# Kernel tuning notes

Hardware: AMD Instinct MI355X
Metric: run time of the kernel (lower is better)

The kernel has to match this reference:

```python
import jax, jax.numpy as jnp
import numpy as np

L, N, D = 4, 50000, 64        # lookback, n_nodes, gnn_dim
E = 500000                    # n_edges
HID = 256
LN_EPS = 1e-5


def setup_inputs() -> dict:
    key = jax.random.key(0)
    ks = jax.random.split(key, 8)
    h_all = jax.random.normal(ks[0], (L, N, D), dtype=jnp.float32)
    src = jax.random.randint(ks[1], (E,), 0, N, dtype=jnp.int32)
    dst = jax.random.randint(ks[2], (E,), 0, N, dtype=jnp.int32)
    W1 = jax.random.normal(ks[3], (HID, L * 2 * D), dtype=jnp.float32) * (1.0 / np.sqrt(L * 2 * D))
    b1 = jax.random.normal(ks[4], (HID,), dtype=jnp.float32) * 0.01
    W3 = jax.random.normal(ks[5], (1, HID), dtype=jnp.float32) * (1.0 / np.sqrt(HID))
    b3 = jax.random.normal(ks[6], (1,), dtype=jnp.float32) * 0.01
    gamma2 = jnp.ones((HID,), dtype=jnp.float32)
    beta2 = jnp.zeros((HID,), dtype=jnp.float32)
    return {"h_all": h_all, "src": src, "dst": dst, "W1": W1, "b1": b1,
            "W3": W3, "b3": b3, "gamma2": gamma2, "beta2": beta2}


def reference(h_all, src, dst, W1, b1, W3, b3, gamma2, beta2):
    lb, _, d = h_all.shape
    # importance weights 1..L normalized
    imp = jnp.arange(1, lb + 1, dtype=h_all.dtype)
    imp = imp / imp.sum()
    # per-edge gather of src/dst features for every lookback step: [L, E, 2D]
    hs = h_all[:, src]                                  # [L, E, D]
    hd = h_all[:, dst]                                  # [L, E, D]
    embed = jnp.concatenate([hs, hd], axis=-1) * imp[:, None, None]
    # concat over lookback steps -> [E, L*2D]
    embed = jnp.transpose(embed, (1, 0, 2)).reshape(embed.shape[1], -1)
    # MLP: W1(tanh) -> LayerNorm -> dropout(eval=identity) -> relu -> W3
    x = jnp.tanh(embed) @ W1.T + b1                     # [E, HID]
    mu = jnp.mean(x, axis=-1, keepdims=True)
    var = jnp.var(x, axis=-1, keepdims=True)
    x = (x - mu) * jax.lax.rsqrt(var + LN_EPS) * gamma2 + beta2
    x = jax.nn.relu(x)
    out = x @ W3.T + b3                                 # [E, 1]
    return out[:, 0]
```

## Files before the change

kernel.cpp:

```cpp
#include <hip/hip_runtime.h>
#include <hip/hip_bf16.h>

#define LL 4
#define NN 50000
#define DD 64
#define EE 500000
#define HID 256
#define KDIM 512
#define LN_EPS 1e-5f

typedef __bf16 bf16x8 __attribute__((ext_vector_type(8)));
typedef float f32x16 __attribute__((ext_vector_type(16)));

__device__ __forceinline__ void async16(const void* g, void* l) {
    __builtin_amdgcn_global_load_lds(
        (const __attribute__((address_space(1))) void*)g,
        (__attribute__((address_space(3))) void*)l, 16, 0, 0);
}

template<int CTRL>
__device__ __forceinline__ float dpp_add(float x) {
    int p = __builtin_amdgcn_update_dpp(0, __builtin_bit_cast(int, x),
                                        CTRL, 0xF, 0xF, true);
    return x + __builtin_bit_cast(float, p);
}

__device__ __forceinline__ float red16(float x) {
    x = dpp_add<0xB1>(x);
    x = dpp_add<0x4E>(x);
    x = dpp_add<0x141>(x);
    x = dpp_add<0x140>(x);
    return x;
}

__global__ void tanh_conv(const float* __restrict__ h, __bf16* __restrict__ t) {
    int i = (blockIdx.x * 256 + threadIdx.x) * 8;
    int l = i / (NN * DD);
    float imp = (float)(l + 1) * 0.1f;
    const float4* p = (const float4*)(h + i);
    float4 a = p[0];
    float4 b = p[1];
    float x[8] = {a.x, a.y, a.z, a.w, b.x, b.y, b.z, b.w};
    bf16x8 r;
    #pragma unroll
    for (int j = 0; j < 8; ++j) {
        float e2 = __expf(2.0f * (imp * x[j]));
        r[j] = (__bf16)(1.0f - 2.0f / (e2 + 1.0f));
    }
    *(bf16x8*)(t + i) = r;
}

__global__ void w2_conv(const float* __restrict__ w1, __bf16* __restrict__ o) {
    int t = blockIdx.x * 256 + threadIdx.x;
    int j  = t & 511;
    int b  = t >> 9;
    int k0 = (b >> 1) * 16 + (b & 1) * 8;
    int r  = j & 255;
    int col = (k0 >> 6) * 128 + ((j >> 8) ? 64 : 0) + (k0 & 63);
    const float4* p = (const float4*)(w1 + r * KDIM + col);
    float4 va = p[0];
    float4 vb = p[1];
    bf16x8 v;
    v[0] = (__bf16)va.x; v[1] = (__bf16)va.y; v[2] = (__bf16)va.z; v[3] = (__bf16)va.w;
    v[4] = (__bf16)vb.x; v[5] = (__bf16)vb.y; v[6] = (__bf16)vb.z; v[7] = (__bf16)vb.w;
    *(bf16x8*)(o + (size_t)t * 8) = v;
}

__global__ __launch_bounds__(256, 2)
void node_proj(const __bf16* __restrict__ tb, const __bf16* __restrict__ w2c,
               const float* __restrict__ b1, __bf16* __restrict__ P) {
    __shared__ __align__(16) char smem[65536];
    __bf16* Bs = (__bf16*)smem;
    float*  Cs = (float*)smem;

    const int tid  = threadIdx.x;
    const int wave = tid >> 6;
    const int lane = tid & 63;
    const int h32  = lane >> 5;
    const int c32  = lane & 31;
    const int cb   = blockIdx.y;
    const int n00  = blockIdx.x * 128;

    #pragma unroll
    for (int it = 0; it < 16; ++it) {
        int o = it * 2048 + tid * 8;
        async16(w2c + (size_t)(o >> 10) * 4096 + cb * 1024 + (o & 1023), Bs + o);
    }

    float badd[8];
    {
        int c0 = (tid * 8) & 127;
        if (cb >= 2) {
            const float4* pb = (const float4*)(b1 + (cb - 2) * 128 + c0);
            float4 u = pb[0], v = pb[1];
            badd[0] = u.x; badd[1] = u.y; badd[2] = u.z; badd[3] = u.w;
            badd[4] = v.x; badd[5] = v.y; badd[6] = v.z; badd[7] = v.w;
        } else {
            #pragma unroll
            for (int z = 0; z < 8; ++z) badd[z] = 0.f;
        }
    }

    int node = n00 + wave * 32 + c32;
    if (node >= NN) node = NN - 1;
    uint4 a[16];
    #pragma unroll
    for (int u = 0; u < 16; ++u) {
        const __bf16* p = tb + (size_t)(u >> 2) * (NN * DD) + node * DD
                        + (u & 3) * 16 + h32 * 8;
        a[u] = *(const uint4*)p;
    }

    f32x16 acc[4];
    #pragma unroll
    for (int nt = 0; nt < 4; ++nt) acc[nt] = (f32x16)(0.f);

    __syncthreads();

    #pragma unroll
    for (int u = 0; u < 16; ++u) {
        bf16x8 af = __builtin_bit_cast(bf16x8, a[u]);
        const __bf16* Bk = Bs + (u * 2 + h32) * 1024 + c32 * 8;
        #pragma unroll
        for (int nt = 0; nt < 4; ++nt) {
            bf16x8 bf = *(const bf16x8*)(Bk + nt * 256);
            acc[nt] = __builtin_amdgcn_mfma_f32_32x32x16_bf16(af, bf, acc[nt], 0, 0, 0);
        }
    }
    __syncthreads();

    #pragma unroll
    for (int nt = 0; nt < 4; ++nt) {
        #pragma unroll
        for (int r = 0; r < 16; ++r) {
            int nl = wave * 32 + (r & 3) + 8 * (r >> 2) + 4 * h32;
            Cs[nl * 128 + nt * 32 + c32] = acc[nt][r];
        }
    }
    __syncthreads();
    #pragma unroll
    for (int it = 0; it < 8; ++it) {
        int o  = it * 2048 + tid * 8;
        int nl = o >> 7;
        int n  = n00 + nl;
        if (n < NN) {
            bf16x8 v;
            #pragma unroll
            for (int z = 0; z < 8; ++z) v[z] = (__bf16)(Cs[o + z] + badd[z]);
            *(bf16x8*)(P + (size_t)n * 512 + cb * 128 + (o & 127)) = v;
        }
    }
}

__global__ __launch_bounds__(256, 3)
void edge_out(const __bf16* __restrict__ P, const int* __restrict__ src,
              const int* __restrict__ dst,
              const float* __restrict__ w3, const float* __restrict__ b3,
              const float* __restrict__ gamma, const float* __restrict__ beta,
              float* __restrict__ out) {
    const int tid = threadIdx.x;
    const int g   = tid >> 4;
    const int j   = tid & 15;

    float gv[16], btv[16], wv[16];
    {
        const float4* pg = (const float4*)(gamma + j * 16);
        const float4* pt = (const float4*)(beta + j * 16);
        const float4* pw = (const float4*)(w3 + j * 16);
        #pragma unroll
        for (int z = 0; z < 4; ++z) {
            float4 vg = pg[z], vt = pt[z], vw = pw[z];
            gv [z*4+0] = vg.x; gv [z*4+1] = vg.y; gv [z*4+2] = vg.z; gv [z*4+3] = vg.w;
            btv[z*4+0] = vt.x; btv[z*4+1] = vt.y; btv[z*4+2] = vt.z; btv[z*4+3] = vt.w;
            wv [z*4+0] = vw.x; wv [z*4+1] = vw.y; wv [z*4+2] = vw.z; wv [z*4+3] = vw.w;
        }
    }
    #pragma unroll
    for (int z = 0; z < 16; ++z) {
        asm volatile("" : "+v"(gv[z]));
        asm volatile("" : "+v"(btv[z]));
        asm volatile("" : "+v"(wv[z]));
    }
    const float b3v = b3[0];
    const int e0 = blockIdx.x * 128 + g * 8;

    int se[8], de[8];
    if (e0 + 8 <= EE) {
        int4 sa = *(const int4*)(src + e0);
        int4 sb = *(const int4*)(src + e0 + 4);
        int4 da = *(const int4*)(dst + e0);
        int4 db = *(const int4*)(dst + e0 + 4);
        se[0]=sa.x; se[1]=sa.y; se[2]=sa.z; se[3]=sa.w;
        se[4]=sb.x; se[5]=sb.y; se[6]=sb.z; se[7]=sb.w;
        de[0]=da.x; de[1]=da.y; de[2]=da.z; de[3]=da.w;
        de[4]=db.x; de[5]=db.y; de[6]=db.z; de[7]=db.w;
    } else {
        #pragma unroll
        for (int z = 0; z < 8; ++z) {
            int ec = e0 + z; if (ec >= EE) ec = EE - 1;
            se[z] = src[ec]; de[z] = dst[ec];
        }
    }

    uint4 s0[3], s1[3], d0[3], d1[3];

    #pragma unroll
    for (int i = 0; i < 2; ++i) {
        const uint4* ps = (const uint4*)(P + (size_t)se[i] * 512 + j * 16);
        const uint4* pd = (const uint4*)(P + (size_t)de[i] * 512 + 256 + j * 16);
        s0[i] = ps[0]; s1[i] = ps[1]; d0[i] = pd[0]; d1[i] = pd[1];
    }

    #pragma unroll
    for (int i = 0; i < 8; ++i) {
        if (i + 2 < 8) {
            const int slot = (i + 2) % 3;
            const uint4* ps = (const uint4*)(P + (size_t)se[i+2] * 512 + j * 16);
            const uint4* pd = (const uint4*)(P + (size_t)de[i+2] * 512 + 256 + j * 16);
            s0[slot] = ps[0]; s1[slot] = ps[1]; d0[slot] = pd[0]; d1[slot] = pd[1];
        }
        const int cs = i % 3;
        bf16x8 a0 = __builtin_bit_cast(bf16x8, s0[cs]);
        bf16x8 a1 = __builtin_bit_cast(bf16x8, s1[cs]);
        bf16x8 c0 = __builtin_bit_cast(bf16x8, d0[cs]);
        bf16x8 c1 = __builtin_bit_cast(bf16x8, d1[cs]);
        float x[16];
        #pragma unroll
        for (int z = 0; z < 8; ++z) {
            x[z]     = (float)a0[z] + (float)c0[z];
            x[z + 8] = (float)a1[z] + (float)c1[z];
        }
        float sum = 0.f, sq = 0.f;
        #pragma unroll
        for (int z = 0; z < 16; ++z) {
            sum += x[z];
            sq   = fmaf(x[z], x[z], sq);
        }
        sum = red16(sum);
        sq  = red16(sq);
        float mu = sum * (1.0f / 256.0f);
        float rs = rsqrtf(sq * (1.0f / 256.0f) - mu * mu + LN_EPS);
        float dot = 0.f;
        #pragma unroll
        for (int z = 0; z < 16; ++z) {
            float y = fmaxf((x[z] - mu) * rs * gv[z] + btv[z], 0.f);
            dot = fmaf(y, wv[z], dot);
        }
        dot = red16(dot);
        int e = e0 + i;
        if (j == 0 && e < EE) out[e] = dot + b3v;
    }
}

extern "C" void kernel_launch(void* const* d_in, const int* in_sizes, int n_in,
                              void* d_out, int out_size, void* d_ws, size_t ws_size,
                              hipStream_t stream) {
    const float* h_all  = (const float*)d_in[0];
    const int*   src    = (const int*)  d_in[1];
    const int*   dst    = (const int*)  d_in[2];
    const float* W1     = (const float*)d_in[3];
    const float* b1     = (const float*)d_in[4];
    const float* W3     = (const float*)d_in[5];
    const float* b3     = (const float*)d_in[6];
    const float* gamma2 = (const float*)d_in[7];
    const float* beta2  = (const float*)d_in[8];
    float* out = (float*)d_out;

    __bf16* tb  = (__bf16*)d_ws;
    __bf16* w2c = tb + (size_t)LL * NN * DD;
    __bf16* P   = w2c + 131072;

    tanh_conv<<<6250, 256, 0, stream>>>(h_all, tb);
    w2_conv<<<64, 256, 0, stream>>>(W1, w2c);
    node_proj<<<dim3((NN + 127) / 128, 4), 256, 0, stream>>>(tb, w2c, b1, P);
    edge_out<<<(EE + 127) / 128, 256, 0, stream>>>(P, src, dst, W3, b3,
                                                   gamma2, beta2, out);
}
```

Before: 201.8 us.

## Bucket edges by source node and remap workgroups per XCD for gather locality

Adds a counting-sort pass (zero, histogram, scan, atomic scatter) that groups edges into 64-node source buckets, reusing the freed tanh buffer as scratch. edge_out then reads the permuted src/dst/edge-id arrays and writes results back through the edge id. It also remaps blockIdx so each XCD handles a contiguous range of work. The aim is better L2 reuse of the projected node rows P during the random gathers, at the cost of four extra small launches, extra index traffic and scattered output stores.

```diff
diff --git a/kernel.cpp b/kernel.cpp
--- a/kernel.cpp
+++ b/kernel.cpp
@@ -8,6 +8,7 @@
 #define HID 256
 #define KDIM 512
 #define LN_EPS 1e-5f
+#define NBK 1024
 
 typedef __bf16 bf16x8 __attribute__((ext_vector_type(8)));
 typedef float f32x16 __attribute__((ext_vector_type(16)));
@@ -24,7 +25,6 @@
                                         CTRL, 0xF, 0xF, true);
     return x + __builtin_bit_cast(float, p);
 }
-
 __device__ __forceinline__ float red16(float x) {
     x = dpp_add<0xB1>(x);
     x = dpp_add<0x4E>(x);
@@ -152,9 +152,65 @@
     }
 }
 
+__global__ __launch_bounds__(1024) void eb_zero(int* __restrict__ cnt) {
+    cnt[threadIdx.x] = 0;
+}
+
+__global__ __launch_bounds__(256) void eb_hist(const int* __restrict__ src,
+                                               int* __restrict__ cnt) {
+    __shared__ int h[NBK];
+    for (int i = threadIdx.x; i < NBK; i += 256) h[i] = 0;
+    __syncthreads();
+    int base = blockIdx.x * 2048 + threadIdx.x * 8;
+    #pragma unroll
+    for (int z = 0; z < 8; ++z) {
+        int e = base + z;
+        if (e < EE) atomicAdd(&h[src[e] >> 6], 1);
+    }
+    __syncthreads();
+    for (int i = threadIdx.x; i < NBK; i += 256)
+        if (h[i]) atomicAdd(&cnt[i], h[i]);
+}
+
+__global__ __launch_bounds__(1024) void eb_scan(const int* __restrict__ cnt,
+                                                int* __restrict__ offs) {
+    __shared__ int s[NBK];
+    int t = threadIdx.x;
+    int my = cnt[t];
+    s[t] = my;
+    __syncthreads();
+    for (int d = 1; d < NBK; d <<= 1) {
+        int v = (t >= d) ? s[t - d] : 0;
+        __syncthreads();
+        s[t] += v;
+        __syncthreads();
+    }
+    offs[t] = s[t] - my;
+}
+
+__global__ __launch_bounds__(256) void eb_scatter(const int* __restrict__ src,
+                                                  const int* __restrict__ dst,
+                                                  int* __restrict__ offs,
+                                                  int* __restrict__ srcp,
+                                                  int* __restrict__ dstp,
+                                                  int* __restrict__ eidp) {
+    int base = blockIdx.x * 2048 + threadIdx.x * 8;
+    #pragma unroll
+    for (int z = 0; z < 8; ++z) {
+        int e = base + z;
+        if (e < EE) {
+            int s = src[e];
+            int pos = atomicAdd(&offs[s >> 6], 1);
+            srcp[pos] = s;
+            dstp[pos] = dst[e];
+            eidp[pos] = e;
+        }
+    }
+}
+
 __global__ __launch_bounds__(256, 3)
-void edge_out(const __bf16* __restrict__ P, const int* __restrict__ src,
-              const int* __restrict__ dst,
+void edge_out(const __bf16* __restrict__ P, const int* __restrict__ srcp,
+              const int* __restrict__ dstp, const int* __restrict__ eidp,
               const float* __restrict__ w3, const float* __restrict__ b3,
               const float* __restrict__ gamma, const float* __restrict__ beta,
               float* __restrict__ out) {
@@ -162,6 +218,11 @@
     const int g   = tid >> 4;
     const int j   = tid & 15;
 
+    const int nwg = (EE + 127) / 128;
+    const int q = nwg >> 3, r = nwg & 7;
+    int xcd = blockIdx.x & 7, idx = blockIdx.x >> 3;
+    int wg = (xcd < r ? xcd * (q + 1) : r * (q + 1) + (xcd - r) * q) + idx;
+
     float gv[16], btv[16], wv[16];
     {
         const float4* pg = (const float4*)(gamma + j * 16);
@@ -175,30 +236,28 @@
             wv [z*4+0] = vw.x; wv [z*4+1] = vw.y; wv [z*4+2] = vw.z; wv [z*4+3] = vw.w;
         }
     }
-    #pragma unroll
-    for (int z = 0; z < 16; ++z) {
-        asm volatile("" : "+v"(gv[z]));
-        asm volatile("" : "+v"(btv[z]));
-        asm volatile("" : "+v"(wv[z]));
-    }
     const float b3v = b3[0];
-    const int e0 = blockIdx.x * 128 + g * 8;
-
-    int se[8], de[8];
+    const int e0 = wg * 128 + g * 8;
+
+    int se[8], de[8], ee[8];
     if (e0 + 8 <= EE) {
-        int4 sa = *(const int4*)(src + e0);
-        int4 sb = *(const int4*)(src + e0 + 4);
-        int4 da = *(const int4*)(dst + e0);
-        int4 db = *(const int4*)(dst + e0 + 4);
+        int4 sa = *(const int4*)(srcp + e0);
+        int4 sb = *(const int4*)(srcp + e0 + 4);
+        int4 da = *(const int4*)(dstp + e0);
+        int4 db = *(const int4*)(dstp + e0 + 4);
+        int4 ea = *(const int4*)(eidp + e0);
+        int4 eb = *(const int4*)(eidp + e0 + 4);
         se[0]=sa.x; se[1]=sa.y; se[2]=sa.z; se[3]=sa.w;
         se[4]=sb.x; se[5]=sb.y; se[6]=sb.z; se[7]=sb.w;
         de[0]=da.x; de[1]=da.y; de[2]=da.z; de[3]=da.w;
         de[4]=db.x; de[5]=db.y; de[6]=db.z; de[7]=db.w;
+        ee[0]=ea.x; ee[1]=ea.y; ee[2]=ea.z; ee[3]=ea.w;
+        ee[4]=eb.x; ee[5]=eb.y; ee[6]=eb.z; ee[7]=eb.w;
     } else {
         #pragma unroll
         for (int z = 0; z < 8; ++z) {
             int ec = e0 + z; if (ec >= EE) ec = EE - 1;
-            se[z] = src[ec]; de[z] = dst[ec];
+            se[z] = srcp[ec]; de[z] = dstp[ec]; ee[z] = eidp[ec];
         }
     }
 
@@ -248,7 +307,7 @@
         }
         dot = red16(dot);
         int e = e0 + i;
-        if (j == 0 && e < EE) out[e] = dot + b3v;
+        if (j == 0 && e < EE) out[ee[i]] = dot + b3v;
     }
 }
 
@@ -270,9 +329,21 @@
     __bf16* w2c = tb + (size_t)LL * NN * DD;
     __bf16* P   = w2c + 131072;
 
+    int* srcp = (int*)tb;
+    int* dstp = srcp + EE;
+    int* eidp = dstp + EE;
+    int* cnt  = eidp + EE;
+    int* offs = cnt + NBK;
+
+    const int nsb = (EE + 2047) / 2048;
+
     tanh_conv<<<6250, 256, 0, stream>>>(h_all, tb);
     w2_conv<<<64, 256, 0, stream>>>(W1, w2c);
     node_proj<<<dim3((NN + 127) / 128, 4), 256, 0, stream>>>(tb, w2c, b1, P);
-    edge_out<<<(EE + 127) / 128, 256, 0, stream>>>(P, src, dst, W3, b3,
-                                                   gamma2, beta2, out);
-}
+    eb_zero<<<1, NBK, 0, stream>>>(cnt);
+    eb_hist<<<nsb, 256, 0, stream>>>(src, cnt);
+    eb_scan<<<1, NBK, 0, stream>>>(cnt, offs);
+    eb_scatter<<<nsb, 256, 0, stream>>>(src, dst, offs, srcp, dstp, eidp);
+    edge_out<<<(EE + 127) / 128, 256, 0, stream>>>(P, srcp, dstp, eidp,
+                                                   W3, b3, gamma2, beta2, out);
+}
```

After: 318.9 us. 1.58x slower.

## Fuse tanh conversion into node projection and loop over column blocks

Applied to the files above, without the earlier changes.

Removes the separate tanh_conv kernel: node_proj now reads fp32 h_all directly, applies the importance-scaled tanh in registers, and keeps the A fragments for all four 128-column blocks. Each block loops over the column blocks, reloading the weight slice into LDS, instead of launching a 4x grid that re-reads the inputs. It also stages the output as bf16 in LDS. This drops a kernel launch and the bf16 intermediate round trip. The cost is fewer blocks (391 instead of 1564), which may not fill the GPU, and weight loads that are serialized inside each block.

```diff
diff --git a/kernel.cpp b/kernel.cpp
--- a/kernel.cpp
+++ b/kernel.cpp
@@ -24,30 +24,12 @@
                                         CTRL, 0xF, 0xF, true);
     return x + __builtin_bit_cast(float, p);
 }
-
 __device__ __forceinline__ float red16(float x) {
     x = dpp_add<0xB1>(x);
     x = dpp_add<0x4E>(x);
     x = dpp_add<0x141>(x);
     x = dpp_add<0x140>(x);
     return x;
-}
-
-__global__ void tanh_conv(const float* __restrict__ h, __bf16* __restrict__ t) {
-    int i = (blockIdx.x * 256 + threadIdx.x) * 8;
-    int l = i / (NN * DD);
-    float imp = (float)(l + 1) * 0.1f;
-    const float4* p = (const float4*)(h + i);
-    float4 a = p[0];
-    float4 b = p[1];
-    float x[8] = {a.x, a.y, a.z, a.w, b.x, b.y, b.z, b.w};
-    bf16x8 r;
-    #pragma unroll
-    for (int j = 0; j < 8; ++j) {
-        float e2 = __expf(2.0f * (imp * x[j]));
-        r[j] = (__bf16)(1.0f - 2.0f / (e2 + 1.0f));
-    }
-    *(bf16x8*)(t + i) = r;
 }
 
 __global__ void w2_conv(const float* __restrict__ w1, __bf16* __restrict__ o) {
@@ -67,87 +49,95 @@
 }
 
 __global__ __launch_bounds__(256, 2)
-void node_proj(const __bf16* __restrict__ tb, const __bf16* __restrict__ w2c,
+void node_proj(const float* __restrict__ h, const __bf16* __restrict__ w2c,
                const float* __restrict__ b1, __bf16* __restrict__ P) {
     __shared__ __align__(16) char smem[65536];
-    __bf16* Bs = (__bf16*)smem;
-    float*  Cs = (float*)smem;
+    __bf16* Bs  = (__bf16*)smem;
+    __bf16* Cs2 = (__bf16*)smem;
 
     const int tid  = threadIdx.x;
     const int wave = tid >> 6;
     const int lane = tid & 63;
     const int h32  = lane >> 5;
     const int c32  = lane & 31;
-    const int cb   = blockIdx.y;
     const int n00  = blockIdx.x * 128;
 
     #pragma unroll
     for (int it = 0; it < 16; ++it) {
         int o = it * 2048 + tid * 8;
-        async16(w2c + (size_t)(o >> 10) * 4096 + cb * 1024 + (o & 1023), Bs + o);
-    }
-
-    float badd[8];
-    {
-        int c0 = (tid * 8) & 127;
-        if (cb >= 2) {
-            const float4* pb = (const float4*)(b1 + (cb - 2) * 128 + c0);
-            float4 u = pb[0], v = pb[1];
-            badd[0] = u.x; badd[1] = u.y; badd[2] = u.z; badd[3] = u.w;
-            badd[4] = v.x; badd[5] = v.y; badd[6] = v.z; badd[7] = v.w;
-        } else {
-            #pragma unroll
-            for (int z = 0; z < 8; ++z) badd[z] = 0.f;
-        }
+        async16(w2c + (size_t)(o >> 10) * 4096 + (o & 1023), Bs + o);
     }
 
     int node = n00 + wave * 32 + c32;
     if (node >= NN) node = NN - 1;
-    uint4 a[16];
+    bf16x8 af[16];
     #pragma unroll
     for (int u = 0; u < 16; ++u) {
-        const __bf16* p = tb + (size_t)(u >> 2) * (NN * DD) + node * DD
-                        + (u & 3) * 16 + h32 * 8;
-        a[u] = *(const uint4*)p;
-    }
-
-    f32x16 acc[4];
-    #pragma unroll
-    for (int nt = 0; nt < 4; ++nt) acc[nt] = (f32x16)(0.f);
-
-    __syncthreads();
-
-    #pragma unroll
-    for (int u = 0; u < 16; ++u) {
-        bf16x8 af = __builtin_bit_cast(bf16x8, a[u]);
-        const __bf16* Bk = Bs + (u * 2 + h32) * 1024 + c32 * 8;
+        int l = u >> 2;
+        float imp = (float)(l + 1) * 0.1f;
+        const float* p = h + (size_t)l * (NN * DD) + node * DD
+                       + (u & 3) * 16 + h32 * 8;
+        float4 va = *(const float4*)p;
+        float4 vb = *(const float4*)(p + 4);
+        float xv[8] = {va.x, va.y, va.z, va.w, vb.x, vb.y, vb.z, vb.w};
+        #pragma unroll
+        for (int z = 0; z < 8; ++z) {
+            float e2 = __expf(2.0f * (imp * xv[z]));
+            af[u][z] = (__bf16)(1.0f - 2.0f / (e2 + 1.0f));
+        }
+    }
+
+    for (int cb = 0; cb < 4; ++cb) {
+        __syncthreads();
+
+        f32x16 acc[4];
+        #pragma unroll
+        for (int nt = 0; nt < 4; ++nt) acc[nt] = (f32x16)(0.f);
+
+        #pragma unroll
+        for (int u = 0; u < 16; ++u) {
+            const __bf16* Bk = Bs + (u * 2 + h32) * 1024 + c32 * 8;
+            #pragma unroll
+            for (int nt = 0; nt < 4; ++nt) {
+                bf16x8 bf = *(const bf16x8*)(Bk + nt * 256);
+                acc[nt] = __builtin_amdgcn_mfma_f32_32x32x16_bf16(af[u], bf, acc[nt], 0, 0, 0);
+            }
+        }
+        __syncthreads();
+
+        float b1v[4];
+        #pragma unroll
+        for (int nt = 0; nt < 4; ++nt)
+            b1v[nt] = (cb >= 2) ? b1[(cb - 2) * 128 + nt * 32 + c32] : 0.f;
+
         #pragma unroll
         for (int nt = 0; nt < 4; ++nt) {
-            bf16x8 bf = *(const bf16x8*)(Bk + nt * 256);
-            acc[nt] = __builtin_amdgcn_mfma_f32_32x32x16_bf16(af, bf, acc[nt], 0, 0, 0);
-        }
-    }
-    __syncthreads();
-
-    #pragma unroll
-    for (int nt = 0; nt < 4; ++nt) {
-        #pragma unroll
-        for (int r = 0; r < 16; ++r) {
-            int nl = wave * 32 + (r & 3) + 8 * (r >> 2) + 4 * h32;
-            Cs[nl * 128 + nt * 32 + c32] = acc[nt][r];
-        }
-    }
-    __syncthreads();
-    #pragma unroll
-    for (int it = 0; it < 8; ++it) {
-        int o  = it * 2048 + tid * 8;
-        int nl = o >> 7;
-        int n  = n00 + nl;
-        if (n < NN) {
-            bf16x8 v;
             #pragma unroll
-            for (int z = 0; z < 8; ++z) v[z] = (__bf16)(Cs[o + z] + badd[z]);
-            *(bf16x8*)(P + (size_t)n * 512 + cb * 128 + (o & 127)) = v;
+            for (int r = 0; r < 16; ++r) {
+                int nl = wave * 32 + (r & 3) + 8 * (r >> 2) + 4 * h32;
+                Cs2[nl * 128 + nt * 32 + c32] = (__bf16)(acc[nt][r] + b1v[nt]);
+            }
+        }
+        __syncthreads();
+
+        #pragma unroll
+        for (int it = 0; it < 8; ++it) {
+            int o  = it * 2048 + tid * 8;
+            int nl = o >> 7;
+            int n  = n00 + nl;
+            if (n < NN)
+                *(bf16x8*)(P + (size_t)n * 512 + cb * 128 + (o & 127)) =
+                    *(const bf16x8*)(Cs2 + o);
+        }
+
+        if (cb < 3) {
+            __syncthreads();
+            #pragma unroll
+            for (int it = 0; it < 16; ++it) {
+                int o = it * 2048 + tid * 8;
+                async16(w2c + (size_t)(o >> 10) * 4096 + (cb + 1) * 1024 + (o & 1023),
+                        Bs + o);
+            }
         }
     }
 }
@@ -266,13 +256,11 @@
     const float* beta2  = (const float*)d_in[8];
     float* out = (float*)d_out;
 
-    __bf16* tb  = (__bf16*)d_ws;
-    __bf16* w2c = tb + (size_t)LL * NN * DD;
+    __bf16* w2c = (__bf16*)d_ws;
     __bf16* P   = w2c + 131072;
 
-    tanh_conv<<<6250, 256, 0, stream>>>(h_all, tb);
     w2_conv<<<64, 256, 0, stream>>>(W1, w2c);
-    node_proj<<<dim3((NN + 127) / 128, 4), 256, 0, stream>>>(tb, w2c, b1, P);
+    node_proj<<<(NN + 127) / 128, 256, 0, stream>>>(h_all, w2c, b1, P);
     edge_out<<<(EE + 127) / 128, 256, 0, stream>>>(P, src, dst, W3, b3,
                                                    gamma2, beta2, out);
 }
```

Result: faster. 195.1 us (-3.4%).
